# Performance work log

Measured on AMD Instinct MI355X. Metric: run time of the kernel, lower is better.

The kernel has to match this reference:

```python
import jax, jax.numpy as jnp
import numpy as np

ROWS, COLS, FEAT = 128, 128, 256
BATCH = 2048


def setup_inputs() -> dict:
    key = jax.random.key(0)
    kx, kw = jax.random.split(key)
    x = jax.random.normal(kx, (BATCH, FEAT), dtype=jnp.float32)
    weights = jax.random.normal(kw, (ROWS, COLS, FEAT), dtype=jnp.float32)
    return {"x": x, "weights": weights}


def reference(x, weights):
    """SOM forward: pairwise Euclidean distance x vs all neurons + BMU argmin.

    x:       [B, S]
    weights: [rows, cols, S]
    returns (distances [B, rows, cols], bmus [B, 2])
    """
    rows, cols, s = weights.shape
    w = weights.reshape(rows * cols, s)                      # [W, S]
    # |a-b|^2 = |a|^2 + |b|^2 - 2 a.b  (avoids the O(B*W*S) repeat of the original)
    d2 = (
        jnp.sum(x * x, axis=-1)[:, None]
        + jnp.sum(w * w, axis=-1)[None, :]
        - 2.0 * (x @ w.T)
    )                                                        # [B, W]
    d = jnp.sqrt(jnp.maximum(d2, 0.0))
    distances = d.reshape(x.shape[0], rows, cols)            # [B, rows, cols]
    min_idx = jnp.argmin(d, axis=-1)                         # [B]
    bmus = jnp.stack((min_idx // cols, min_idx % cols), axis=1)  # [B, 2]
    return distances, bmus
```

## Files before the change

### kernel.cpp

```cpp
#include <hip/hip_runtime.h>
#include <math.h>

#define BATCH 2048
#define NW    16384
#define FEAT  256
#define SOMC  128
#define BM    128
#define BN    128
#define KTILES 8
#define SPLITK 512

typedef __attribute__((ext_vector_type(8)))  short short8v;
typedef __attribute__((ext_vector_type(16))) float f32x16;

#define WS_NEEDED 18964480ull

static __device__ __forceinline__ unsigned short f2bf(float f) {
    unsigned u = __float_as_uint(f);
    unsigned r = u + 0x7FFFu + ((u >> 16) & 1u);
    return (unsigned short)(r >> 16);
}

static __device__ __forceinline__ void gload16(const void* g, void* l) {
    __builtin_amdgcn_global_load_lds(
        (const __attribute__((address_space(1))) unsigned int*)g,
        (__attribute__((address_space(3))) unsigned int*)l, 16, 0, 0);
}

__global__ __launch_bounds__(256) void som_prep_split(const float* __restrict__ x,
                                                      const float* __restrict__ w,
                                                      float* __restrict__ xn,
                                                      float* __restrict__ wn,
                                                      unsigned long long* __restrict__ bmu,
                                                      unsigned short* __restrict__ xsp,
                                                      unsigned short* __restrict__ wsp) {
    const int wv = threadIdx.x >> 6;
    const int lane = threadIdx.x & 63;
    const int row = blockIdx.x * 4 + wv;
    const bool isx = row < BATCH;
    const float* src = isx ? x + (size_t)row * FEAT
                           : w + (size_t)(row - BATCH) * FEAT;
    float4 v = ((const float4*)src)[lane];
    float s = v.x * v.x + v.y * v.y + v.z * v.z + v.w * v.w;
    #pragma unroll
    for (int o = 32; o; o >>= 1) s += __shfl_xor(s, o, 64);

    float fx[4] = {v.x, v.y, v.z, v.w};
    unsigned short h[4], l[4];
    #pragma unroll
    for (int i = 0; i < 4; ++i) {
        h[i] = f2bf(fx[i]);
        float hf = __uint_as_float((unsigned)h[i] << 16);
        l[i] = f2bf(fx[i] - hf);
    }
    unsigned short* dst = isx ? xsp + (size_t)row * SPLITK
                              : wsp + (size_t)(row - BATCH) * SPLITK;
    const int k = lane * 4;
    const int base = (k >> 5) * 64 + (k & 31);
    *(ushort4*)(dst + base)      = make_ushort4(h[0], h[1], h[2], h[3]);
    *(ushort4*)(dst + base + 32) = make_ushort4(l[0], l[1], l[2], l[3]);

    if (lane == 0) {
        if (isx) { xn[row] = s; bmu[row] = 0xFFFFFFFFFFFFFFFFULL; }
        else     { wn[row - BATCH] = s; }
    }
}

__global__ __launch_bounds__(256, 4) void som_mfma(const unsigned short* __restrict__ xsp,
                                                   const unsigned short* __restrict__ wsp,
                                                   const float* __restrict__ xn,
                                                   const float* __restrict__ wn,
                                                   float* __restrict__ out,
                                                   unsigned long long* __restrict__ bmu) {
    __shared__ __align__(16) char xsb[128 * 128];
    __shared__ __align__(16) char wsb[128 * 128];

    const int t = threadIdx.x;
    const int brow = blockIdx.y * BM;
    const int bcol = blockIdx.x * BN;
    const int lane = t & 63, wv = t >> 6;
    const int wrow = (wv >> 1) * 64;
    const int wcol = (wv & 1) * 64;
    const int c32 = lane & 31, q5 = lane >> 5;

    const int srow   = wv * 32 + (lane >> 3);
    const int schunk = (lane & 7) ^ (lane >> 3);
    const unsigned short* gx = xsp + (size_t)(brow + srow) * SPLITK + schunk * 8;
    const unsigned short* gw = wsp + (size_t)(bcol + srow) * SPLITK + schunk * 8;
    char* lx = xsb + (wv * 32) * 128;
    char* lw = wsb + (wv * 32) * 128;

    f32x16 zz;
    #pragma unroll
    for (int i = 0; i < 16; ++i) zz[i] = 0.0f;
    f32x16 acc00 = zz, acc01 = zz, acc10 = zz, acc11 = zz;

    #pragma unroll
    for (int kt = 0; kt < KTILES; ++kt) {
        #pragma unroll
        for (int j = 0; j < 4; ++j) {
            gload16(gx + (size_t)j * 8 * SPLITK + kt * 64, lx + j * 1024);
            gload16(gw + (size_t)j * 8 * SPLITK + kt * 64, lw + j * 1024);
        }
        __syncthreads();

        #pragma unroll
        for (int ks = 0; ks < 2; ++ks) {
            const int hiB = ks * 32 + q5 * 16;
            const int loB = 64 + ks * 32 + q5 * 16;
            #define LDF(buf, r, gc) (*(const short8v*)((buf) + (r) * 128 + ((gc) ^ (((r) & 7) << 4))))
            const int ra0 = wrow + c32, ra1 = wrow + 32 + c32;
            const int rb0 = wcol + c32, rb1 = wcol + 32 + c32;
            short8v ah0 = LDF(xsb, ra0, hiB), ah1 = LDF(xsb, ra1, hiB);
            short8v al0 = LDF(xsb, ra0, loB), al1 = LDF(xsb, ra1, loB);
            short8v bh0 = LDF(wsb, rb0, hiB), bh1 = LDF(wsb, rb1, hiB);
            short8v bl0 = LDF(wsb, rb0, loB), bl1 = LDF(wsb, rb1, loB);
            #undef LDF
            acc00 = __builtin_amdgcn_mfma_f32_32x32x16_bf16(ah0, bh0, acc00, 0, 0, 0);
            acc01 = __builtin_amdgcn_mfma_f32_32x32x16_bf16(ah0, bh1, acc01, 0, 0, 0);
            acc10 = __builtin_amdgcn_mfma_f32_32x32x16_bf16(ah1, bh0, acc10, 0, 0, 0);
            acc11 = __builtin_amdgcn_mfma_f32_32x32x16_bf16(ah1, bh1, acc11, 0, 0, 0);
            acc00 = __builtin_amdgcn_mfma_f32_32x32x16_bf16(ah0, bl0, acc00, 0, 0, 0);
            acc01 = __builtin_amdgcn_mfma_f32_32x32x16_bf16(ah0, bl1, acc01, 0, 0, 0);
            acc10 = __builtin_amdgcn_mfma_f32_32x32x16_bf16(ah1, bl0, acc10, 0, 0, 0);
            acc11 = __builtin_amdgcn_mfma_f32_32x32x16_bf16(ah1, bl1, acc11, 0, 0, 0);
            acc00 = __builtin_amdgcn_mfma_f32_32x32x16_bf16(al0, bh0, acc00, 0, 0, 0);
            acc01 = __builtin_amdgcn_mfma_f32_32x32x16_bf16(al0, bh1, acc01, 0, 0, 0);
            acc10 = __builtin_amdgcn_mfma_f32_32x32x16_bf16(al1, bh0, acc10, 0, 0, 0);
            acc11 = __builtin_amdgcn_mfma_f32_32x32x16_bf16(al1, bh1, acc11, 0, 0, 0);
        }
        __syncthreads();
    }

    #pragma unroll
    for (int m = 0; m < 2; ++m) {
        const f32x16 a0 = m ? acc10 : acc00;
        const f32x16 a1 = m ? acc11 : acc01;
        #pragma unroll
        for (int reg = 0; reg < 16; ++reg) {
            const int rg = brow + wrow + m * 32 + (reg & 3) + 8 * (reg >> 2) + 4 * q5;
            const float xv = xn[rg];
            unsigned long long best = 0xFFFFFFFFFFFFFFFFULL;
            #pragma unroll
            for (int n = 0; n < 2; ++n) {
                const int cg = bcol + wcol + n * 32 + c32;
                const float dot = n ? a1[reg] : a0[reg];
                float d2 = fmaxf(xv + wn[cg] - 2.0f * dot, 0.0f);
                float d = sqrtf(d2);
                out[(size_t)rg * NW + cg] = d;
                unsigned long long p =
                    ((unsigned long long)__float_as_uint(d) << 32) | (unsigned)cg;
                if (p < best) best = p;
            }
            #pragma unroll
            for (int o = 16; o; o >>= 1) {
                unsigned long long ob = __shfl_xor(best, o, 64);
                if (ob < best) best = ob;
            }
            if (c32 == 0) atomicMin(&bmu[rg], best);
        }
    }
}

#define BK  32
#define LDK 36

__global__ __launch_bounds__(256) void som_prep(const float* __restrict__ x,
                                                const float* __restrict__ w,
                                                float* __restrict__ xn,
                                                float* __restrict__ wn,
                                                unsigned long long* __restrict__ bmu) {
    const int wave = threadIdx.x >> 6;
    const int lane = threadIdx.x & 63;
    const int row  = blockIdx.x * 4 + wave;
    const float* src = (row < BATCH) ? (x + (size_t)row * FEAT)
                                     : (w + (size_t)(row - BATCH) * FEAT);
    float4 v = ((const float4*)src)[lane];
    float s = v.x * v.x + v.y * v.y + v.z * v.z + v.w * v.w;
    #pragma unroll
    for (int off = 32; off >= 1; off >>= 1) s += __shfl_xor(s, off, 64);
    if (lane == 0) {
        if (row < BATCH) { xn[row] = s; bmu[row] = 0xFFFFFFFFFFFFFFFFULL; }
        else             { wn[row - BATCH] = s; }
    }
}

__global__ __launch_bounds__(256) void som_f32main(const float* __restrict__ x,
                                                   const float* __restrict__ w,
                                                   const float* __restrict__ xn,
                                                   const float* __restrict__ wn,
                                                   float* __restrict__ out,
                                                   unsigned long long* __restrict__ bmu) {
    __shared__ float xs[BM][LDK];
    __shared__ float wsh[BN][LDK];
    const int t  = threadIdx.x;
    const int tx = t & 15;
    const int ty = t >> 4;
    const int brow = blockIdx.y * BM;
    const int bcol = blockIdx.x * BN;
    float acc[8][8];
    #pragma unroll
    for (int i = 0; i < 8; ++i)
        #pragma unroll
        for (int j = 0; j < 8; ++j) acc[i][j] = 0.0f;
    for (int k0 = 0; k0 < FEAT; k0 += BK) {
        #pragma unroll
        for (int r = 0; r < 4; ++r) {
            const int flat = (t + r * 256) * 4;
            const int row  = flat >> 5;
            const int col  = flat & 31;
            float4 xv = *(const float4*)&x[(size_t)(brow + row) * FEAT + k0 + col];
            float4 wv = *(const float4*)&w[(size_t)(bcol + row) * FEAT + k0 + col];
            *(float4*)&xs[row][col]  = xv;
            *(float4*)&wsh[row][col] = wv;
        }
        __syncthreads();
        #pragma unroll
        for (int kq = 0; kq < BK / 4; ++kq) {
            float4 a[8], b[8];
            #pragma unroll
            for (int i = 0; i < 8; ++i) a[i] = *(const float4*)&xs[ty + 16 * i][kq * 4];
            #pragma unroll
            for (int j = 0; j < 8; ++j) b[j] = *(const float4*)&wsh[tx + 16 * j][kq * 4];
            #pragma unroll
            for (int i = 0; i < 8; ++i)
                #pragma unroll
                for (int j = 0; j < 8; ++j) {
                    acc[i][j] += a[i].x * b[j].x;
                    acc[i][j] += a[i].y * b[j].y;
                    acc[i][j] += a[i].z * b[j].z;
                    acc[i][j] += a[i].w * b[j].w;
                }
        }
        __syncthreads();
    }
    #pragma unroll
    for (int i = 0; i < 8; ++i) {
        const int rg = brow + ty + 16 * i;
        const float xnv = xn[rg];
        unsigned long long best = 0xFFFFFFFFFFFFFFFFULL;
        #pragma unroll
        for (int j = 0; j < 8; ++j) {
            const int cg = bcol + tx + 16 * j;
            float d2 = xnv + wn[cg] - 2.0f * acc[i][j];
            d2 = fmaxf(d2, 0.0f);
            float d = sqrtf(d2);
            out[(size_t)rg * NW + cg] = d;
            unsigned long long p =
                ((unsigned long long)__float_as_uint(d) << 32) | (unsigned int)cg;
            if (p < best) best = p;
        }
        #pragma unroll
        for (int off = 8; off >= 1; off >>= 1) {
            unsigned long long o = __shfl_xor(best, off, 64);
            if (o < best) best = o;
        }
        if (tx == 0) atomicMin(&bmu[rg], best);
    }
}

__global__ __launch_bounds__(256) void som_bmu_write(const unsigned long long* __restrict__ bmu,
                                                     float* __restrict__ outb) {
    const int i = blockIdx.x * blockDim.x + threadIdx.x;
    if (i >= BATCH) return;
    const unsigned int idx = (unsigned int)(bmu[i] & 0xFFFFFFFFu);
    outb[(size_t)i * 2 + 0] = (float)(idx >> 7);
    outb[(size_t)i * 2 + 1] = (float)(idx & (SOMC - 1));
}

extern "C" void kernel_launch(void* const* d_in, const int* in_sizes, int n_in,
                              void* d_out, int out_size, void* d_ws, size_t ws_size,
                              hipStream_t stream) {
    const float* x = (const float*)d_in[0];
    const float* w = (const float*)d_in[1];
    float* out = (float*)d_out;

    float* xn = (float*)d_ws;
    float* wn = xn + BATCH;
    unsigned long long* bmu = (unsigned long long*)((char*)d_ws + 73728);
    float* outb = out + (size_t)BATCH * NW;

    if (ws_size >= WS_NEEDED) {
        unsigned short* xsp = (unsigned short*)((char*)d_ws + 90112);
        unsigned short* wsp = (unsigned short*)((char*)d_ws + 2187264);
        som_prep_split<<<(BATCH + NW) / 4, 256, 0, stream>>>(x, w, xn, wn, bmu, xsp, wsp);
        dim3 grid(NW / BN, BATCH / BM);
        som_mfma<<<grid, 256, 0, stream>>>(xsp, wsp, xn, wn, out, bmu);
    } else {
        som_prep<<<(BATCH + NW) / 4, 256, 0, stream>>>(x, w, xn, wn, bmu);
        dim3 grid(NW / BN, BATCH / BM);
        som_f32main<<<grid, 256, 0, stream>>>(x, w, xn, wn, out, bmu);
    }
    som_bmu_write<<<(BATCH + 255) / 256, 256, 0, stream>>>(bmu, outb);
}
```

Measured before the change: 141.8 us.

## Double-buffer LDS tiles and remap block order for L2 locality

Adds double-buffered LDS staging so the global-to-LDS loads for the next k-tile are issued before computing the current one. This replaces the load-then-barrier serialization and removes one barrier per iteration. It also remaps block indices so that groups of consecutive blocks share tiles, aiming at better L2 reuse, and precomputes the swizzle. LDS use doubles and launch bounds drop from 4 to 2 blocks per CU, which may reduce occupancy for the store-heavy epilogue.

New measurement: 147.8 us. 4.3% more time.

```diff
diff --git a/kernel.cpp b/kernel.cpp
--- a/kernel.cpp
+++ b/kernel.cpp
@@ -66,71 +66,102 @@
     }
 }
 
-__global__ __launch_bounds__(256, 4) void som_mfma(const unsigned short* __restrict__ xsp,
+__global__ __launch_bounds__(256, 2) void som_mfma(const unsigned short* __restrict__ xsp,
                                                    const unsigned short* __restrict__ wsp,
                                                    const float* __restrict__ xn,
                                                    const float* __restrict__ wn,
                                                    float* __restrict__ out,
                                                    unsigned long long* __restrict__ bmu) {
-    __shared__ __align__(16) char xsb[128 * 128];
-    __shared__ __align__(16) char wsb[128 * 128];
+    __shared__ __align__(16) char xsb[2][16384];
+    __shared__ __align__(16) char wsb[2][16384];
+
+    const int disp = blockIdx.y * gridDim.x + blockIdx.x;
+    const int work = (disp & 7) * 256 + (disp >> 3);
+    const int bcol = (work >> 4) * BN;
+    const int brow = (work & 15) * BM;
 
     const int t = threadIdx.x;
-    const int brow = blockIdx.y * BM;
-    const int bcol = blockIdx.x * BN;
     const int lane = t & 63, wv = t >> 6;
     const int wrow = (wv >> 1) * 64;
     const int wcol = (wv & 1) * 64;
     const int c32 = lane & 31, q5 = lane >> 5;
-
-    const int srow   = wv * 32 + (lane >> 3);
-    const int schunk = (lane & 7) ^ (lane >> 3);
-    const unsigned short* gx = xsp + (size_t)(brow + srow) * SPLITK + schunk * 8;
-    const unsigned short* gw = wsp + (size_t)(bcol + srow) * SPLITK + schunk * 8;
-    char* lx = xsb + (wv * 32) * 128;
-    char* lw = wsb + (wv * 32) * 128;
+    const int rsw = ((c32 & 7) ^ (c32 >> 3)) << 4;
+
+    const unsigned short* gxj[4];
+    const unsigned short* gwj[4];
+    #pragma unroll
+    for (int j = 0; j < 4; ++j) {
+        const int r  = wv * 32 + j * 8 + (lane >> 3);
+        const int sc = (lane & 7) ^ (lane >> 3) ^ j;
+        gxj[j] = xsp + (size_t)(brow + r) * SPLITK + sc * 8;
+        gwj[j] = wsp + (size_t)(bcol + r) * SPLITK + sc * 8;
+    }
+    const int ldsoff = (wv * 32) * 128;
+
+#define STAGE(kt, b) do {                                                   \
+        char* lx_ = xsb[b] + ldsoff;                                        \
+        char* lw_ = wsb[b] + ldsoff;                                        \
+        _Pragma("unroll")                                                   \
+        for (int j_ = 0; j_ < 4; ++j_) {                                    \
+            gload16(gxj[j_] + (kt) * 64, lx_ + j_ * 1024);                  \
+            gload16(gwj[j_] + (kt) * 64, lw_ + j_ * 1024);                  \
+        }                                                                   \
+    } while (0)
 
     f32x16 zz;
     #pragma unroll
     for (int i = 0; i < 16; ++i) zz[i] = 0.0f;
     f32x16 acc00 = zz, acc01 = zz, acc10 = zz, acc11 = zz;
 
-    #pragma unroll
-    for (int kt = 0; kt < KTILES; ++kt) {
-        #pragma unroll
-        for (int j = 0; j < 4; ++j) {
-            gload16(gx + (size_t)j * 8 * SPLITK + kt * 64, lx + j * 1024);
-            gload16(gw + (size_t)j * 8 * SPLITK + kt * 64, lw + j * 1024);
-        }
-        __syncthreads();
-
-        #pragma unroll
-        for (int ks = 0; ks < 2; ++ks) {
-            const int hiB = ks * 32 + q5 * 16;
-            const int loB = 64 + ks * 32 + q5 * 16;
-            #define LDF(buf, r, gc) (*(const short8v*)((buf) + (r) * 128 + ((gc) ^ (((r) & 7) << 4))))
-            const int ra0 = wrow + c32, ra1 = wrow + 32 + c32;
-            const int rb0 = wcol + c32, rb1 = wcol + 32 + c32;
-            short8v ah0 = LDF(xsb, ra0, hiB), ah1 = LDF(xsb, ra1, hiB);
-            short8v al0 = LDF(xsb, ra0, loB), al1 = LDF(xsb, ra1, loB);
-            short8v bh0 = LDF(wsb, rb0, hiB), bh1 = LDF(wsb, rb1, hiB);
-            short8v bl0 = LDF(wsb, rb0, loB), bl1 = LDF(wsb, rb1, loB);
-            #undef LDF
-            acc00 = __builtin_amdgcn_mfma_f32_32x32x16_bf16(ah0, bh0, acc00, 0, 0, 0);
-            acc01 = __builtin_amdgcn_mfma_f32_32x32x16_bf16(ah0, bh1, acc01, 0, 0, 0);
-            acc10 = __builtin_amdgcn_mfma_f32_32x32x16_bf16(ah1, bh0, acc10, 0, 0, 0);
-            acc11 = __builtin_amdgcn_mfma_f32_32x32x16_bf16(ah1, bh1, acc11, 0, 0, 0);
-            acc00 = __builtin_amdgcn_mfma_f32_32x32x16_bf16(ah0, bl0, acc00, 0, 0, 0);
-            acc01 = __builtin_amdgcn_mfma_f32_32x32x16_bf16(ah0, bl1, acc01, 0, 0, 0);
-            acc10 = __builtin_amdgcn_mfma_f32_32x32x16_bf16(ah1, bl0, acc10, 0, 0, 0);
-            acc11 = __builtin_amdgcn_mfma_f32_32x32x16_bf16(ah1, bl1, acc11, 0, 0, 0);
-            acc00 = __builtin_amdgcn_mfma_f32_32x32x16_bf16(al0, bh0, acc00, 0, 0, 0);
-            acc01 = __builtin_amdgcn_mfma_f32_32x32x16_bf16(al0, bh1, acc01, 0, 0, 0);
-            acc10 = __builtin_amdgcn_mfma_f32_32x32x16_bf16(al1, bh0, acc10, 0, 0, 0);
-            acc11 = __builtin_amdgcn_mfma_f32_32x32x16_bf16(al1, bh1, acc11, 0, 0, 0);
-        }
-        __syncthreads();
-    }
+    const int ra0 = wrow + c32, ra1 = wrow + 32 + c32;
+    const int rb0 = wcol + c32, rb1 = wcol + 32 + c32;
+
+#define LDF(buf, r, gc) (*(const short8v*)((buf) + (r) * 128 + ((gc) ^ rsw)))
+#define COMPUTE(b) do {                                                         \
+        const char* xb_ = xsb[b];                                               \
+        const char* wb_ = wsb[b];                                               \
+        _Pragma("unroll")                                                       \
+        for (int ks = 0; ks < 2; ++ks) {                                        \
+            const int hiB = ks * 32 + q5 * 16;                                  \
+            const int loB = 64 + hiB;                                           \
+            short8v ah0 = LDF(xb_, ra0, hiB), ah1 = LDF(xb_, ra1, hiB);         \
+            short8v al0 = LDF(xb_, ra0, loB), al1 = LDF(xb_, ra1, loB);         \
+            short8v bh0 = LDF(wb_, rb0, hiB), bh1 = LDF(wb_, rb1, hiB);         \
+            short8v bl0 = LDF(wb_, rb0, loB), bl1 = LDF(wb_, rb1, loB);         \
+            acc00 = __builtin_amdgcn_mfma_f32_32x32x16_bf16(ah0, bh0, acc00, 0, 0, 0); \
+            acc01 = __builtin_amdgcn_mfma_f32_32x32x16_bf16(ah0, bh1, acc01, 0, 0, 0); \
+            acc10 = __builtin_amdgcn_mfma_f32_32x32x16_bf16(ah1, bh0, acc10, 0, 0, 0); \
+            acc11 = __builtin_amdgcn_mfma_f32_32x32x16_bf16(ah1, bh1, acc11, 0, 0, 0); \
+            acc00 = __builtin_amdgcn_mfma_f32_32x32x16_bf16(ah0, bl0, acc00, 0, 0, 0); \
+            acc01 = __builtin_amdgcn_mfma_f32_32x32x16_bf16(ah0, bl1, acc01, 0, 0, 0); \
+            acc10 = __builtin_amdgcn_mfma_f32_32x32x16_bf16(ah1, bl0, acc10, 0, 0, 0); \
+            acc11 = __builtin_amdgcn_mfma_f32_32x32x16_bf16(ah1, bl1, acc11, 0, 0, 0); \
+            acc00 = __builtin_amdgcn_mfma_f32_32x32x16_bf16(al0, bh0, acc00, 0, 0, 0); \
+            acc01 = __builtin_amdgcn_mfma_f32_32x32x16_bf16(al0, bh1, acc01, 0, 0, 0); \
+            acc10 = __builtin_amdgcn_mfma_f32_32x32x16_bf16(al1, bh0, acc10, 0, 0, 0); \
+            acc11 = __builtin_amdgcn_mfma_f32_32x32x16_bf16(al1, bh1, acc11, 0, 0, 0); \
+        }                                                                       \
+    } while (0)
+
+    STAGE(0, 0);
+    asm volatile("s_waitcnt vmcnt(0)" ::: "memory");
+    __builtin_amdgcn_s_barrier();
+    asm volatile("" ::: "memory");
+
+    #pragma unroll
+    for (int kt = 0; kt < KTILES - 1; ++kt) {
+        const int cur = kt & 1;
+        STAGE(kt + 1, cur ^ 1);
+        COMPUTE(cur);
+        asm volatile("s_waitcnt vmcnt(0)" ::: "memory");
+        __builtin_amdgcn_s_barrier();
+        asm volatile("" ::: "memory");
+    }
+    COMPUTE((KTILES - 1) & 1);
+
+#undef STAGE
+#undef LDF
+#undef COMPUTE
 
     #pragma unroll
     for (int m = 0; m < 2; ++m) {
```

## Pre-pack bf16 split operands in MFMA fragment order and load directly from global

Applied to the files above, without the earlier changes.

The prep kernel now writes the hi/lo bf16 split of x and weights in a layout that matches the per-lane MFMA operand fragments, 32-row panels with each lane's 8 elements contiguous. The MFMA kernel drops the LDS staging buffers and both __syncthreads per K-tile and reads fragments straight from global memory with 16-byte vector loads. The distance output now uses nontemporal stores. This removes LDS traffic and barriers, but operand loads lose cross-wave sharing through LDS, and global load latency is no longer hidden by a staged pipeline.

New measurement: 143.3 us. About the same (+1.0%).

```diff
diff --git a/kernel.cpp b/kernel.cpp
--- a/kernel.cpp
+++ b/kernel.cpp
@@ -15,16 +15,11 @@
 
 #define WS_NEEDED 18964480ull
 
+
 static __device__ __forceinline__ unsigned short f2bf(float f) {
     unsigned u = __float_as_uint(f);
     unsigned r = u + 0x7FFFu + ((u >> 16) & 1u);
     return (unsigned short)(r >> 16);
-}
-
-static __device__ __forceinline__ void gload16(const void* g, void* l) {
-    __builtin_amdgcn_global_load_lds(
-        (const __attribute__((address_space(1))) unsigned int*)g,
-        (__attribute__((address_space(3))) unsigned int*)l, 16, 0, 0);
 }
 
 __global__ __launch_bounds__(256) void som_prep_split(const float* __restrict__ x,
@@ -32,8 +27,8 @@
                                                       float* __restrict__ xn,
                                                       float* __restrict__ wn,
                                                       unsigned long long* __restrict__ bmu,
-                                                      unsigned short* __restrict__ xsp,
-                                                      unsigned short* __restrict__ wsp) {
+                                                      unsigned short* __restrict__ xf,
+                                                      unsigned short* __restrict__ wf) {
     const int wv = threadIdx.x >> 6;
     const int lane = threadIdx.x & 63;
     const int row = blockIdx.x * 4 + wv;
@@ -53,12 +48,15 @@
         float hf = __uint_as_float((unsigned)h[i] << 16);
         l[i] = f2bf(fx[i] - hf);
     }
-    unsigned short* dst = isx ? xsp + (size_t)row * SPLITK
-                              : wsp + (size_t)(row - BATCH) * SPLITK;
-    const int k = lane * 4;
-    const int base = (k >> 5) * 64 + (k & 31);
-    *(ushort4*)(dst + base)      = make_ushort4(h[0], h[1], h[2], h[3]);
-    *(ushort4*)(dst + base + 32) = make_ushort4(l[0], l[1], l[2], l[3]);
+    const int lr = isx ? row : row - BATCH;
+    const int k  = lane * 4;
+    const int kt = k >> 5, ko = k & 31;
+    const int ks = ko >> 4, q5 = (ko >> 3) & 1, e = ko & 7;
+    unsigned short* base = (isx ? xf : wf)
+        + (size_t)(lr >> 5) * 16384 + (size_t)kt * 2048
+        + ks * 512 + q5 * 256 + (lr & 31) * 8 + e;
+    *(ushort4*)(base)        = make_ushort4(h[0], h[1], h[2], h[3]);
+    *(ushort4*)(base + 1024) = make_ushort4(l[0], l[1], l[2], l[3]);
 
     if (lane == 0) {
         if (isx) { xn[row] = s; bmu[row] = 0xFFFFFFFFFFFFFFFFULL; }
@@ -66,29 +64,25 @@
     }
 }
 
-__global__ __launch_bounds__(256, 4) void som_mfma(const unsigned short* __restrict__ xsp,
-                                                   const unsigned short* __restrict__ wsp,
+__global__ __launch_bounds__(256, 4) void som_mfma(const unsigned short* __restrict__ xf,
+                                                   const unsigned short* __restrict__ wf,
                                                    const float* __restrict__ xn,
                                                    const float* __restrict__ wn,
                                                    float* __restrict__ out,
                                                    unsigned long long* __restrict__ bmu) {
-    __shared__ __align__(16) char xsb[128 * 128];
-    __shared__ __align__(16) char wsb[128 * 128];
-
-    const int t = threadIdx.x;
     const int brow = blockIdx.y * BM;
     const int bcol = blockIdx.x * BN;
+
+    const int t = threadIdx.x;
     const int lane = t & 63, wv = t >> 6;
     const int wrow = (wv >> 1) * 64;
     const int wcol = (wv & 1) * 64;
     const int c32 = lane & 31, q5 = lane >> 5;
 
-    const int srow   = wv * 32 + (lane >> 3);
-    const int schunk = (lane & 7) ^ (lane >> 3);
-    const unsigned short* gx = xsp + (size_t)(brow + srow) * SPLITK + schunk * 8;
-    const unsigned short* gw = wsp + (size_t)(bcol + srow) * SPLITK + schunk * 8;
-    char* lx = xsb + (wv * 32) * 128;
-    char* lw = wsb + (wv * 32) * 128;
+    const unsigned short* A0 = xf + (size_t)((brow + wrow) >> 5) * 16384 + lane * 8;
+    const unsigned short* A1 = A0 + 16384;
+    const unsigned short* B0 = wf + (size_t)((bcol + wcol) >> 5) * 16384 + lane * 8;
+    const unsigned short* B1 = B0 + 16384;
 
     f32x16 zz;
     #pragma unroll
@@ -97,25 +91,19 @@
 
     #pragma unroll
     for (int kt = 0; kt < KTILES; ++kt) {
-        #pragma unroll
-        for (int j = 0; j < 4; ++j) {
-            gload16(gx + (size_t)j * 8 * SPLITK + kt * 64, lx + j * 1024);
-            gload16(gw + (size_t)j * 8 * SPLITK + kt * 64, lw + j * 1024);
-        }
-        __syncthreads();
-
+        const int kb = kt * 2048;
         #pragma unroll
         for (int ks = 0; ks < 2; ++ks) {
-            const int hiB = ks * 32 + q5 * 16;
-            const int loB = 64 + ks * 32 + q5 * 16;
-            #define LDF(buf, r, gc) (*(const short8v*)((buf) + (r) * 128 + ((gc) ^ (((r) & 7) << 4))))
-            const int ra0 = wrow + c32, ra1 = wrow + 32 + c32;
-            const int rb0 = wcol + c32, rb1 = wcol + 32 + c32;
-            short8v ah0 = LDF(xsb, ra0, hiB), ah1 = LDF(xsb, ra1, hiB);
-            short8v al0 = LDF(xsb, ra0, loB), al1 = LDF(xsb, ra1, loB);
-            short8v bh0 = LDF(wsb, rb0, hiB), bh1 = LDF(wsb, rb1, hiB);
-            short8v bl0 = LDF(wsb, rb0, loB), bl1 = LDF(wsb, rb1, loB);
-            #undef LDF
+            const int hb = kb + ks * 512;
+            const int lb = hb + 1024;
+            short8v ah0 = *(const short8v*)(A0 + hb);
+            short8v ah1 = *(const short8v*)(A1 + hb);
+            short8v al0 = *(const short8v*)(A0 + lb);
+            short8v al1 = *(const short8v*)(A1 + lb);
+            short8v bh0 = *(const short8v*)(B0 + hb);
+            short8v bh1 = *(const short8v*)(B1 + hb);
+            short8v bl0 = *(const short8v*)(B0 + lb);
+            short8v bl1 = *(const short8v*)(B1 + lb);
             acc00 = __builtin_amdgcn_mfma_f32_32x32x16_bf16(ah0, bh0, acc00, 0, 0, 0);
             acc01 = __builtin_amdgcn_mfma_f32_32x32x16_bf16(ah0, bh1, acc01, 0, 0, 0);
             acc10 = __builtin_amdgcn_mfma_f32_32x32x16_bf16(ah1, bh0, acc10, 0, 0, 0);
@@ -129,7 +117,6 @@
             acc10 = __builtin_amdgcn_mfma_f32_32x32x16_bf16(al1, bh0, acc10, 0, 0, 0);
             acc11 = __builtin_amdgcn_mfma_f32_32x32x16_bf16(al1, bh1, acc11, 0, 0, 0);
         }
-        __syncthreads();
     }
 
     #pragma unroll
@@ -147,7 +134,7 @@
                 const float dot = n ? a1[reg] : a0[reg];
                 float d2 = fmaxf(xv + wn[cg] - 2.0f * dot, 0.0f);
                 float d = sqrtf(d2);
-                out[(size_t)rg * NW + cg] = d;
+                __builtin_nontemporal_store(d, &out[(size_t)rg * NW + cg]);
                 unsigned long long p =
                     ((unsigned long long)__float_as_uint(d) << 32) | (unsigned)cg;
                 if (p < best) best = p;
@@ -281,11 +268,11 @@
     float* outb = out + (size_t)BATCH * NW;
 
     if (ws_size >= WS_NEEDED) {
-        unsigned short* xsp = (unsigned short*)((char*)d_ws + 90112);
-        unsigned short* wsp = (unsigned short*)((char*)d_ws + 2187264);
-        som_prep_split<<<(BATCH + NW) / 4, 256, 0, stream>>>(x, w, xn, wn, bmu, xsp, wsp);
+        unsigned short* xf = (unsigned short*)((char*)d_ws + 90112);
+        unsigned short* wf = (unsigned short*)((char*)d_ws + 2187264);
+        som_prep_split<<<(BATCH + NW) / 4, 256, 0, stream>>>(x, w, xn, wn, bmu, xf, wf);
         dim3 grid(NW / BN, BATCH / BM);
-        som_mfma<<<grid, 256, 0, stream>>>(xsp, wsp, xn, wn, out, bmu);
+        som_mfma<<<grid, 256, 0, stream>>>(xf, wf, xn, wn, out, bmu);
     } else {
         som_prep<<<(BATCH + NW) / 4, 256, 0, stream>>>(x, w, xn, wn, bmu);
         dim3 grid(NW / BN, BATCH / BM);
```
